# Kernel tuning notes

Hardware: AMD Instinct MI355X
Metric: run time of the kernel (lower is better)

## Reference

```python
import jax, jax.numpy as jnp
import numpy as np

SHIFT = 1  # fixed choice for the random +/-1 shift_direction in the torch module


def setup_inputs() -> dict:
    key = jax.random.key(0)
    kx, kw = jax.random.split(key)
    x = jax.random.normal(kx, (128, 128, 56, 56), dtype=jnp.float32)
    W = jax.random.normal(kw, (32, 3, 2, 3, 4), dtype=jnp.float32)
    return {"x": x, "W": W}


def reference(x, W):
    n = x.shape[0]
    # sum-pool over a factor-2 split of the channel dim: (n,128,56,56)->(n,64,56,56)
    t = x.reshape(n, 2, 64, 56, 56).sum(axis=1)
    # view channels as (32 groups, 2): (n,32,2,56,56)
    t = t.reshape(n, 32, 2, 56, 56)
    # first torch unfold == size-3 zero-padded window along the 32-group axis
    tp = jnp.pad(t, ((0, 0), (1, 1), (0, 0), (0, 0), (0, 0)))
    w1 = jnp.stack([tp[:, i:i + 32] for i in range(3)], axis=1)  # (n,3,32,2,56,56)
    # circular shift along the last spatial axis (torch.roll on dim 5)
    w1 = jnp.roll(w1, SHIFT, axis=5)
    # second torch unfold == size-3 zero-padded window along the rolled 56 axis
    wp = jnp.pad(w1, ((0, 0), (0, 0), (0, 0), (0, 0), (0, 0), (1, 1)))
    w2 = jnp.stack([wp[..., l:l + 56] for l in range(3)], axis=5)  # (n,3,32,2,56,3,56)
    # grouped local-conv contraction; axes: n,i=win1(3),j=32,m=2,p=56,l=win2(3),o=56; k=4
    out = jnp.einsum('nijmplo,jimlk->njpok', w2, W)  # (n,32,56,56,4)
    t5 = out.transpose(0, 2, 3, 1, 4).reshape(n, 56, 56, 128)
    t5 = jnp.roll(t5, SHIFT, axis=1)  # roll along first spatial axis
    return t5.transpose(0, 3, 1, 2)  # (n,128,56,56)
```

## Files before the change

kernel.cpp:

```cpp
#include <hip/hip_runtime.h>

#define TPB 256

__global__ __launch_bounds__(TPB) void fused_shift_conv(const float* __restrict__ x,
                                                        const float* __restrict__ Wg,
                                                        float* __restrict__ out) {
    const int bid = blockIdx.x;
    const int p = bid % 56;
    const int n = bid / 56;
    const int P = (p + 55) % 56;

    __shared__ float sm[64 * 57];

    const int tid = threadIdx.x;
    const int h = tid & 1;
    const int c = tid >> 1;
    const int j = c >> 2;
    const int k = c & 3;

    float wt[3][2][3];
#pragma unroll
    for (int i = 0; i < 3; ++i)
#pragma unroll
        for (int m = 0; m < 2; ++m)
#pragma unroll
            for (int l = 0; l < 3; ++l)
                wt[i][m][l] = Wg[(((j * 3 + i) * 2 + m) * 3 + l) * 4 + k];

    {
        const float4* x4 = reinterpret_cast<const float4*>(x);
#pragma unroll
        for (int it = 0; it < 4; ++it) {
            const int idx = tid + it * TPB;
            if (idx < 896) {
                const int r = idx / 14;
                const int v = idx - r * 14;
                const size_t base = (size_t)(n * 128 + r) * 784 + (size_t)P * 14 + (size_t)v;
                const float4 a = x4[base];
                const float4 b = x4[base + (size_t)64 * 784];
                const int s = r * 57 + v * 4;
                sm[s + 0] = a.x + b.x;
                sm[s + 1] = a.y + b.y;
                sm[s + 2] = a.z + b.z;
                sm[s + 3] = a.w + b.w;
            }
        }
    }
    __syncthreads();

    const int sbase = h * 28 - 2;
    const int sp1 = h ? 27 : 55;

    float acc[28];
#pragma unroll
    for (int u = 0; u < 28; ++u) acc[u] = 0.f;

#pragma unroll
    for (int i = 0; i < 3; ++i) {
        const int g = j + i - 1;
        if ((unsigned)g < 32u) {
#pragma unroll
            for (int m = 0; m < 2; ++m) {
                const float* row = &sm[(2 * g + m) * 57];
                float val[30];
                const float v26 = row[26];
                const float v27 = row[27];
                val[0]  = h ? v26 : 0.f;
                val[1]  = row[sp1];
                val[29] = h ? 0.f : v27;
#pragma unroll
                for (int d = 2; d < 29; ++d) val[d] = row[sbase + d];

                const float w0 = wt[i][m][0];
                const float w1 = wt[i][m][1];
                const float w2 = wt[i][m][2];
#pragma unroll
                for (int u = 0; u < 28; ++u)
                    acc[u] += w0 * val[u] + w1 * val[u + 1] + w2 * val[u + 2];
            }
        }
    }

    const int off = h * 28;
    const int chalf = c >> 6;
    const int crow = c & 63;
    float4* o4 = reinterpret_cast<float4*>(out);

#pragma unroll
    for (int half = 0; half < 2; ++half) {
        __syncthreads();
        if (chalf == half) {
            float* orow = &sm[crow * 57 + off];
#pragma unroll
            for (int u = 0; u < 28; ++u) orow[u] = acc[u];
        }
        __syncthreads();
#pragma unroll
        for (int it = 0; it < 4; ++it) {
            const int idx = tid + it * TPB;
            if (idx < 896) {
                const int r = idx / 14;
                const int v = idx - r * 14;
                const float* s = &sm[r * 57 + v * 4];
                float4 val4;
                val4.x = s[0]; val4.y = s[1]; val4.z = s[2]; val4.w = s[3];
                o4[(size_t)(n * 128 + half * 64 + r) * 784 + (size_t)p * 14 + (size_t)v] = val4;
            }
        }
    }
}

extern "C" void kernel_launch(void* const* d_in, const int* in_sizes, int n_in,
                              void* d_out, int out_size, void* d_ws, size_t ws_size,
                              hipStream_t stream) {
    const float* x = (const float*)d_in[0];
    const float* W = (const float*)d_in[1];
    float* out = (float*)d_out;
    const int n = in_sizes[0] / (128 * 56 * 56);
    const int grid = n * 56;
    fused_shift_conv<<<grid, TPB, 0, stream>>>(x, W, out);
}
```

Before: 116.0 us.

## Process two output rows per block with 512 threads and contiguous row-pair stores

Each block now computes two adjacent output rows p0 and p0+1, using 512 threads split into two 256-thread halves. Weights and indexing are shared, and the grid is halved. The output staging packs both rows per channel so each channel writes 112 contiguous floats as float2 stores, giving longer contiguous write segments. Shared memory doubles to two 64x57 tiles, which may reduce occupancy, and the stores change from float4 to float2.

```diff
diff --git a/kernel.cpp b/kernel.cpp
--- a/kernel.cpp
+++ b/kernel.cpp
@@ -1,20 +1,25 @@
 #include <hip/hip_runtime.h>
 
-#define TPB 256
+#define TPB 512
 
 __global__ __launch_bounds__(TPB) void fused_shift_conv(const float* __restrict__ x,
                                                         const float* __restrict__ Wg,
                                                         float* __restrict__ out) {
     const int bid = blockIdx.x;
-    const int p = bid % 56;
-    const int n = bid / 56;
-    const int P = (p + 55) % 56;
+    const int ptile = bid % 28;
+    const int n = bid / 28;
+    const int p0 = ptile * 2;
 
-    __shared__ float sm[64 * 57];
+    const int P0 = (p0 + 55) % 56;
+    const int P1 = p0;
+
+    __shared__ float sm[2 * 64 * 57];
 
     const int tid = threadIdx.x;
-    const int h = tid & 1;
-    const int c = tid >> 1;
+    const int pl = tid >> 8;
+    const int t8 = tid & 255;
+    const int h = t8 & 1;
+    const int c = t8 >> 1;
     const int j = c >> 2;
     const int k = c & 3;
 
@@ -32,13 +37,16 @@
 #pragma unroll
         for (int it = 0; it < 4; ++it) {
             const int idx = tid + it * TPB;
-            if (idx < 896) {
-                const int r = idx / 14;
-                const int v = idx - r * 14;
-                const size_t base = (size_t)(n * 128 + r) * 784 + (size_t)P * 14 + (size_t)v;
+            if (idx < 1792) {
+                const int r = idx / 28;
+                const int rem = idx - r * 28;
+                const int q = rem / 14;
+                const int v = rem - q * 14;
+                const int Pr = q ? P1 : P0;
+                const size_t base = (size_t)(n * 128 + r) * 784 + (size_t)Pr * 14 + (size_t)v;
                 const float4 a = x4[base];
                 const float4 b = x4[base + (size_t)64 * 784];
-                const int s = r * 57 + v * 4;
+                const int s = (r * 2 + q) * 57 + v * 4;
                 sm[s + 0] = a.x + b.x;
                 sm[s + 1] = a.y + b.y;
                 sm[s + 2] = a.z + b.z;
@@ -61,7 +69,7 @@
         if ((unsigned)g < 32u) {
 #pragma unroll
             for (int m = 0; m < 2; ++m) {
-                const float* row = &sm[(2 * g + m) * 57];
+                const float* row = &sm[((2 * g + m) * 2 + pl) * 57];
                 float val[30];
                 const float v26 = row[26];
                 const float v27 = row[27];
@@ -81,31 +89,29 @@
         }
     }
 
-    const int off = h * 28;
+    const int off = pl * 56 + h * 28;
     const int chalf = c >> 6;
-    const int crow = c & 63;
-    float4* o4 = reinterpret_cast<float4*>(out);
+    const int cr = c & 63;
+    float2* o2 = reinterpret_cast<float2*>(out);
 
 #pragma unroll
     for (int half = 0; half < 2; ++half) {
         __syncthreads();
         if (chalf == half) {
-            float* orow = &sm[crow * 57 + off];
+            float* orow = &sm[cr * 113 + off];
 #pragma unroll
             for (int u = 0; u < 28; ++u) orow[u] = acc[u];
         }
         __syncthreads();
 #pragma unroll
-        for (int it = 0; it < 4; ++it) {
+        for (int it = 0; it < 7; ++it) {
             const int idx = tid + it * TPB;
-            if (idx < 896) {
-                const int r = idx / 14;
-                const int v = idx - r * 14;
-                const float* s = &sm[r * 57 + v * 4];
-                float4 val4;
-                val4.x = s[0]; val4.y = s[1]; val4.z = s[2]; val4.w = s[3];
-                o4[(size_t)(n * 128 + half * 64 + r) * 784 + (size_t)p * 14 + (size_t)v] = val4;
-            }
+            const int ch = idx / 56;
+            const int w2 = idx - ch * 56;
+            float2 v2;
+            v2.x = sm[ch * 113 + 2 * w2];
+            v2.y = sm[ch * 113 + 2 * w2 + 1];
+            o2[(size_t)(n * 128 + half * 64 + ch) * 1568 + (size_t)p0 * 28 + (size_t)w2] = v2;
         }
     }
 }
@@ -117,6 +123,6 @@
     const float* W = (const float*)d_in[1];
     float* out = (float*)d_out;
     const int n = in_sizes[0] / (128 * 56 * 56);
-    const int grid = n * 56;
+    const int grid = n * 28;
     fused_shift_conv<<<grid, TPB, 0, stream>>>(x, W, out);
 }
```

New measurement: 97.09 us. 16.3% less time.

## Remap threads to compute two output channels over 14-column strips

Applied to the files above, without the earlier changes.

Reassigns threads so each computes two adjacent k outputs for one group over a 14-column quarter of the row instead of one output over 28 columns. Each shared-memory value loaded is reused for two weights, the weights are loaded as float2, and fewer registers are live per thread. Launch bounds now request 4 blocks per SIMD-level occupancy. Warp-level divergence on q and the write-back mapping change, which may alter LDS bank conflicts.

```diff
diff --git a/kernel.cpp b/kernel.cpp
--- a/kernel.cpp
+++ b/kernel.cpp
@@ -2,9 +2,9 @@
 
 #define TPB 256
 
-__global__ __launch_bounds__(TPB) void fused_shift_conv(const float* __restrict__ x,
-                                                        const float* __restrict__ Wg,
-                                                        float* __restrict__ out) {
+__global__ __launch_bounds__(TPB, 4) void fused_shift_conv(const float* __restrict__ x,
+                                                           const float* __restrict__ Wg,
+                                                           float* __restrict__ out) {
     const int bid = blockIdx.x;
     const int p = bid % 56;
     const int n = bid / 56;
@@ -13,19 +13,25 @@
     __shared__ float sm[64 * 57];
 
     const int tid = threadIdx.x;
-    const int h = tid & 1;
-    const int c = tid >> 1;
-    const int j = c >> 2;
-    const int k = c & 3;
+    const int j  = tid & 31;
+    const int kp = (tid >> 5) & 1;
+    const int q  = tid >> 6;
+    const int cb = q * 14;
 
-    float wt[3][2][3];
+    float wt[3][2][3][2];
+    {
+        const float2* W2 = reinterpret_cast<const float2*>(Wg);
 #pragma unroll
-    for (int i = 0; i < 3; ++i)
+        for (int i = 0; i < 3; ++i)
 #pragma unroll
-        for (int m = 0; m < 2; ++m)
+            for (int m = 0; m < 2; ++m)
 #pragma unroll
-            for (int l = 0; l < 3; ++l)
-                wt[i][m][l] = Wg[(((j * 3 + i) * 2 + m) * 3 + l) * 4 + k];
+                for (int l = 0; l < 3; ++l) {
+                    const float2 w = W2[(((j * 3 + i) * 2 + m) * 3 + l) * 2 + kp];
+                    wt[i][m][l][0] = w.x;
+                    wt[i][m][l][1] = w.y;
+                }
+    }
 
     {
         const float4* x4 = reinterpret_cast<const float4*>(x);
@@ -48,12 +54,11 @@
     }
     __syncthreads();
 
-    const int sbase = h * 28 - 2;
-    const int sp1 = h ? 27 : 55;
-
-    float acc[28];
+    float acc[2][14];
 #pragma unroll
-    for (int u = 0; u < 28; ++u) acc[u] = 0.f;
+    for (int kk = 0; kk < 2; ++kk)
+#pragma unroll
+        for (int u = 0; u < 14; ++u) acc[kk][u] = 0.f;
 
 #pragma unroll
     for (int i = 0; i < 3; ++i) {
@@ -62,49 +67,58 @@
 #pragma unroll
             for (int m = 0; m < 2; ++m) {
                 const float* row = &sm[(2 * g + m) * 57];
-                float val[30];
-                const float v26 = row[26];
-                const float v27 = row[27];
-                val[0]  = h ? v26 : 0.f;
-                val[1]  = row[sp1];
-                val[29] = h ? 0.f : v27;
+                const float* rowq = row + cb - 2;
+                float val[16];
+                if (q == 0) {
+                    val[0] = 0.f;
+                    val[1] = row[55];
 #pragma unroll
-                for (int d = 2; d < 29; ++d) val[d] = row[sbase + d];
-
-                const float w0 = wt[i][m][0];
-                const float w1 = wt[i][m][1];
-                const float w2 = wt[i][m][2];
+                    for (int d = 2; d < 16; ++d) val[d] = rowq[d];
+                } else {
 #pragma unroll
-                for (int u = 0; u < 28; ++u)
-                    acc[u] += w0 * val[u] + w1 * val[u + 1] + w2 * val[u + 2];
+                    for (int d = 0; d < 16; ++d) val[d] = rowq[d];
+                    if (q == 3) val[15] = 0.f;
+                }
+#pragma unroll
+                for (int l = 0; l < 3; ++l) {
+                    const float w0 = wt[i][m][l][0];
+                    const float w1 = wt[i][m][l][1];
+#pragma unroll
+                    for (int u = 0; u < 14; ++u) {
+                        acc[0][u] += w0 * val[u + l];
+                        acc[1][u] += w1 * val[u + l];
+                    }
+                }
             }
         }
     }
 
-    const int off = h * 28;
-    const int chalf = c >> 6;
-    const int crow = c & 63;
+    const int c0 = j * 4 + kp * 2;
+    const int chalf = c0 >> 6;
     float4* o4 = reinterpret_cast<float4*>(out);
 
 #pragma unroll
     for (int half = 0; half < 2; ++half) {
         __syncthreads();
         if (chalf == half) {
-            float* orow = &sm[crow * 57 + off];
 #pragma unroll
-            for (int u = 0; u < 28; ++u) orow[u] = acc[u];
+            for (int kk = 0; kk < 2; ++kk) {
+                float* orow = &sm[((c0 & 63) + kk) * 57 + cb];
+#pragma unroll
+                for (int u = 0; u < 14; ++u) orow[u] = acc[kk][u];
+            }
         }
         __syncthreads();
 #pragma unroll
         for (int it = 0; it < 4; ++it) {
             const int idx = tid + it * TPB;
             if (idx < 896) {
-                const int r = idx / 14;
-                const int v = idx - r * 14;
-                const float* s = &sm[r * 57 + v * 4];
-                float4 val4;
-                val4.x = s[0]; val4.y = s[1]; val4.z = s[2]; val4.w = s[3];
-                o4[(size_t)(n * 128 + half * 64 + r) * 784 + (size_t)p * 14 + (size_t)v] = val4;
+                const int ch = idx / 14;
+                const int v = idx - ch * 14;
+                const float* s = &sm[ch * 57 + v * 4];
+                float4 v4;
+                v4.x = s[0]; v4.y = s[1]; v4.z = s[2]; v4.w = s[3];
+                o4[(size_t)(n * 128 + half * 64 + ch) * 784 + (size_t)p * 14 + (size_t)v] = v4;
             }
         }
     }
```

New measurement: 121.1 us. +4.4%, slower.
